# Kernel tuning notes

Hardware: AMD Instinct MI355X
Metric: run time of the kernel (lower is better)

Reference implementation:

```python
import jax, jax.numpy as jnp
import numpy as np

NUM_HEADS = 12
OT_REG = 0.1
SINKHORN_ITERS = 10
DIAG_VAL = 1e3


def setup_inputs() -> dict:
    key = jax.random.key(0)
    k1, k2, k3 = jax.random.split(key, 3)
    B, N, C = 64, 256, 768
    x = jax.random.normal(k1, (B, N, C), dtype=jnp.float32)
    w_qkv = jax.random.normal(k2, (3 * C, C), dtype=jnp.float32) * (C ** -0.5)
    w_proj = jax.random.normal(k3, (C, C), dtype=jnp.float32) * (C ** -0.5)
    b_proj = jnp.zeros((C,), dtype=jnp.float32)
    return {"x": x, "w_qkv": w_qkv, "w_proj": w_proj, "b_proj": b_proj}


def _sot(q):
    # q: [B, H, N, hd] -> self-optimal-transport plan [B, H, N, N]
    N = q.shape[-2]
    qn = q / (jnp.linalg.norm(q, axis=-1, keepdims=True) + 1e-8)
    C = 1.0 - jnp.einsum('bhnd,bhmd->bhnm', qn, qn)          # cosine cost
    eye = jnp.eye(N, dtype=bool)
    C = jnp.where(eye, DIAG_VAL, C)                            # mask diagonal
    log_K = -C / OT_REG
    log_marg = -jnp.log(jnp.float32(N))                        # uniform r = c = 1/N
    log_v = jnp.zeros(q.shape[:2] + (N,), dtype=q.dtype)
    for _ in range(SINKHORN_ITERS):
        log_u = log_marg - jax.nn.logsumexp(log_K + log_v[..., None, :], axis=-1)
        log_v = log_marg - jax.nn.logsumexp(log_K + log_u[..., :, None], axis=-2)
    log_T = log_u[..., :, None] + log_K + log_v[..., None, :]
    z = jnp.exp(log_T)
    z = z / jnp.max(z, axis=(-2, -1), keepdims=True)           # max_scale per sample/head
    z = jnp.where(eye, 1.0, z)                                 # diagonal set to 1
    return z


def reference(x, w_qkv, w_proj, b_proj):
    B, N, C = x.shape
    H = NUM_HEADS
    hd = C // H
    scale = hd ** -0.5
    qkv = jnp.einsum('bnc,oc->bno', x, w_qkv)                  # [B, N, 3C]
    qkv = qkv.reshape(B, N, 3, H, hd).transpose(2, 0, 3, 1, 4)  # [3, B, H, N, hd]
    q, k, v = qkv[0], qkv[1], qkv[2]
    attn = _sot(q)                                              # [B, H, N, N]
    attn = jax.nn.softmax(attn * scale, axis=-1)               # dropout = identity (eval)
    out = jnp.einsum('bhnm,bhmd->bhnd', attn, v)
    out = out.transpose(0, 2, 1, 3).reshape(B, N, C)
    out = jnp.einsum('bnc,oc->bno', out, w_proj) + b_proj
    return out
```

## Files before the change

kernel.cpp:

```cpp
#include <hip/hip_runtime.h>

typedef unsigned short u16;
typedef unsigned int   u32;
typedef __attribute__((ext_vector_type(8))) short bf16x8;
typedef __attribute__((ext_vector_type(4))) float f32x4;

__device__ __forceinline__ u16 f2bf(float f) {
    u32 u = __float_as_uint(f);
    u += 0x7fffu + ((u >> 16) & 1u);
    return (u16)(u >> 16);
}
__device__ __forceinline__ float bf2f(u16 s) {
    return __uint_as_float(((u32)s) << 16);
}
__device__ __forceinline__ u32 pack2bf(float f0, float f1) {
    return (u32)f2bf(f0) | ((u32)f2bf(f1) << 16);
}
__device__ __forceinline__ u32 cvtpk2bf(float f0, float f1) {
    u32 r;
    asm("v_cvt_pk_bf16_f32 %0, %1, %2" : "=v"(r) : "v"(f0), "v"(f1));
    return r;
}

__device__ __forceinline__ void gload_lds16(const void* g, void* l) {
    __builtin_amdgcn_global_load_lds(
        (const __attribute__((address_space(1))) u32*)g,
        (__attribute__((address_space(3))) u32*)l, 16, 0, 0);
}

__global__ __launch_bounds__(256)
void conv_all(const float* __restrict__ x, const float* __restrict__ wqkv,
              const float* __restrict__ wproj, u16* __restrict__ xbf,
              u16* __restrict__ wqv, u16* __restrict__ wpb)
{
    const int i = blockIdx.x * 256 + threadIdx.x;
    if (i < 1572864) {
        const float4 a = ((const float4*)x)[2*i];
        const float4 b = ((const float4*)x)[2*i + 1];
        ((uint4*)xbf)[i] = make_uint4(pack2bf(a.x,a.y), pack2bf(a.z,a.w),
                                      pack2bf(b.x,b.y), pack2bf(b.z,b.w));
    } else if (i < 1572864 + 147456) {
        const int j = i - 1572864;
        const int row = j / 96;
        const int cc  = (j - row * 96) * 8;
        const int srow = row + (row >= 768 ? 768 : 0);
        const float4 a = *(const float4*)&wqkv[(size_t)srow*768 + cc];
        const float4 b = *(const float4*)&wqkv[(size_t)srow*768 + cc + 4];
        *(uint4*)&wqv[(size_t)row*768 + cc] =
            make_uint4(pack2bf(a.x,a.y), pack2bf(a.z,a.w),
                       pack2bf(b.x,b.y), pack2bf(b.z,b.w));
    } else if (i < 1572864 + 147456 + 73728) {
        const int j = i - 1572864 - 147456;
        const float4 a = ((const float4*)wproj)[2*j];
        const float4 b = ((const float4*)wproj)[2*j + 1];
        ((uint4*)wpb)[j] = make_uint4(pack2bf(a.x,a.y), pack2bf(a.z,a.w),
                                      pack2bf(b.x,b.y), pack2bf(b.z,b.w));
    }
}

__global__ __launch_bounds__(256, 3)
void gemm_qkv_mfma(const u16* __restrict__ xbf, const u16* __restrict__ wqv,
                   u16* __restrict__ qnbf, u16* __restrict__ vbfT)
{
    __shared__ u16 As[128*64];
    __shared__ u16 Bq[128*64];
    __shared__ u16 Bv[128*64];
    const int m0 = blockIdx.x * 128;
    const int bj = blockIdx.y;
    const int tid = threadIdx.x;
    const int l = tid & 63, w = tid >> 6;
    const int wr = w >> 1, wc = w & 1;

    f32x4 accq[4][4], accv[4][4];
    #pragma unroll
    for (int i = 0; i < 4; ++i)
        #pragma unroll
        for (int j = 0; j < 4; ++j) {
            accq[i][j] = (f32x4){0.f,0.f,0.f,0.f};
            accv[i][j] = (f32x4){0.f,0.f,0.f,0.f};
        }

    const char* Ar  = (const char*)xbf + (size_t)m0*1536;
    const char* Bqr = (const char*)wqv + (size_t)(bj*128)*1536;
    const char* Bvr = (const char*)wqv + (size_t)(768 + bj*128)*1536;
    char* Asb = (char*)As;
    char* Bqb = (char*)Bq;
    char* Bvb = (char*)Bv;
    const int co = 16 * ((l & 7) ^ (l >> 3));
    const size_t rstep = (size_t)(l >> 3) * 1536;
    const int rsw = (l & 7) << 4;

    for (int k0 = 0; k0 < 1536; k0 += 128) {
        #pragma unroll
        for (int i = 0; i < 4; ++i) {
            const int rb = i*32 + w*8;
            const size_t goff = (size_t)rb*1536 + rstep + k0 + co;
            gload_lds16(Ar  + goff, Asb + i*4096 + w*1024);
            gload_lds16(Bqr + goff, Bqb + i*4096 + w*1024);
            gload_lds16(Bvr + goff, Bvb + i*4096 + w*1024);
        }
        __syncthreads();
        #pragma unroll
        for (int kk = 0; kk < 2; ++kk) {
            const int coff = (kk*64 + ((l >> 4) << 4)) ^ rsw;
            bf16x8 af[4], bq[4], bv[4];
            #pragma unroll
            for (int mi = 0; mi < 4; ++mi) {
                const int rowA = wr*64 + mi*16 + (l & 15);
                af[mi] = *(const bf16x8*)(Asb + rowA*128 + coff);
                const int rowB = wc*64 + mi*16 + (l & 15);
                bq[mi] = *(const bf16x8*)(Bqb + rowB*128 + coff);
                bv[mi] = *(const bf16x8*)(Bvb + rowB*128 + coff);
            }
            #pragma unroll
            for (int mi = 0; mi < 4; ++mi)
                #pragma unroll
                for (int nj = 0; nj < 4; ++nj)
                    accq[mi][nj] = __builtin_amdgcn_mfma_f32_16x16x32_bf16(
                                       af[mi], bq[nj], accq[mi][nj], 0, 0, 0);
            #pragma unroll
            for (int mi = 0; mi < 4; ++mi)
                #pragma unroll
                for (int nj = 0; nj < 4; ++nj)
                    accv[mi][nj] = __builtin_amdgcn_mfma_f32_16x16x32_bf16(
                                       af[mi], bv[nj], accv[mi][nj], 0, 0, 0);
        }
        __syncthreads();
    }

    const int rbase = m0 + wr*64 + ((l >> 4) << 2);
    {
        const int h = 2*bj + wc;
        #pragma unroll
        for (int mi = 0; mi < 4; ++mi)
            #pragma unroll
            for (int rr = 0; rr < 4; ++rr) {
                float s =      accq[mi][0][rr]*accq[mi][0][rr];
                s = fmaf(accq[mi][1][rr], accq[mi][1][rr], s);
                s = fmaf(accq[mi][2][rr], accq[mi][2][rr], s);
                s = fmaf(accq[mi][3][rr], accq[mi][3][rr], s);
                #pragma unroll
                for (int off = 1; off < 16; off <<= 1) s += __shfl_xor(s, off);
                const float inv = 1.0f / (sqrtf(s) + 1e-8f);
                const int m = rbase + mi*16 + rr;
                const int b_ = m >> 8, n_ = m & 255;
                u16* row = qnbf + ((((size_t)b_*12 + h) << 8) + n_)*64;
                #pragma unroll
                for (int nj = 0; nj < 4; ++nj)
                    row[nj*16 + (l & 15)] = f2bf(accq[mi][nj][rr] * inv);
            }
    }
    {
        const int colb = bj*128 + wc*64;
        #pragma unroll
        for (int mi = 0; mi < 4; ++mi)
            #pragma unroll
            for (int nj = 0; nj < 4; ++nj) {
                const int col = colb + nj*16 + (l & 15);
                const int h = col >> 6, d = col & 63;
                const int m = rbase + mi*16;
                const int b_ = m >> 8, n_ = m & 255;
                uint2 o = make_uint2(pack2bf(accv[mi][nj][0], accv[mi][nj][1]),
                                     pack2bf(accv[mi][nj][2], accv[mi][nj][3]));
                *(uint2*)&vbfT[(((size_t)b_*12 + h)*64 + d)*256 + n_] = o;
            }
    }
}

__global__ __launch_bounds__(256, 2)
void gemm_proj_mfma(const u16* __restrict__ ctxb, const u16* __restrict__ wpb,
                    const float* __restrict__ bias, float* __restrict__ out)
{
    __shared__ u16 As[128*64];
    __shared__ u16 B1[128*64];
    __shared__ u16 B2[128*64];
    const int m0 = blockIdx.x * 128;
    const int n0 = blockIdx.y * 256;
    const int tid = threadIdx.x;
    const int l = tid & 63, w = tid >> 6;
    const int wr = w >> 1, wc = w & 1;

    f32x4 acc1[4][4], acc2[4][4];
    #pragma unroll
    for (int i = 0; i < 4; ++i)
        #pragma unroll
        for (int j = 0; j < 4; ++j) {
            acc1[i][j] = (f32x4){0.f,0.f,0.f,0.f};
            acc2[i][j] = (f32x4){0.f,0.f,0.f,0.f};
        }

    const char* Ar  = (const char*)ctxb + (size_t)m0*1536;
    const char* B1r = (const char*)wpb + (size_t)n0*1536;
    const char* B2r = (const char*)wpb + (size_t)(n0 + 128)*1536;
    char* Asb = (char*)As;
    char* B1b = (char*)B1;
    char* B2b = (char*)B2;
    const int co = 16 * ((l & 7) ^ (l >> 3));
    const size_t rstep = (size_t)(l >> 3) * 1536;
    const int rsw = (l & 7) << 4;

    for (int k0 = 0; k0 < 1536; k0 += 128) {
        #pragma unroll
        for (int i = 0; i < 4; ++i) {
            const int rb = i*32 + w*8;
            const size_t goff = (size_t)rb*1536 + rstep + k0 + co;
            gload_lds16(Ar  + goff, Asb + i*4096 + w*1024);
            gload_lds16(B1r + goff, B1b + i*4096 + w*1024);
            gload_lds16(B2r + goff, B2b + i*4096 + w*1024);
        }
        __syncthreads();
        #pragma unroll
        for (int kk = 0; kk < 2; ++kk) {
            const int coff = (kk*64 + ((l >> 4) << 4)) ^ rsw;
            bf16x8 af[4], b1[4], b2[4];
            #pragma unroll
            for (int mi = 0; mi < 4; ++mi) {
                const int rowA = wr*64 + mi*16 + (l & 15);
                af[mi] = *(const bf16x8*)(Asb + rowA*128 + coff);
                const int rowB = wc*64 + mi*16 + (l & 15);
                b1[mi] = *(const bf16x8*)(B1b + rowB*128 + coff);
                b2[mi] = *(const bf16x8*)(B2b + rowB*128 + coff);
            }
            #pragma unroll
            for (int mi = 0; mi < 4; ++mi)
                #pragma unroll
                for (int nj = 0; nj < 4; ++nj)
                    acc1[mi][nj] = __builtin_amdgcn_mfma_f32_16x16x32_bf16(
                                       af[mi], b1[nj], acc1[mi][nj], 0, 0, 0);
            #pragma unroll
            for (int mi = 0; mi < 4; ++mi)
                #pragma unroll
                for (int nj = 0; nj < 4; ++nj)
                    acc2[mi][nj] = __builtin_amdgcn_mfma_f32_16x16x32_bf16(
                                       af[mi], b2[nj], acc2[mi][nj], 0, 0, 0);
        }
        __syncthreads();
    }

    const int rbase = m0 + wr*64 + ((l >> 4) << 2);
    #pragma unroll
    for (int mi = 0; mi < 4; ++mi)
        #pragma unroll
        for (int nj = 0; nj < 4; ++nj) {
            const int col = n0 + wc*64 + nj*16 + (l & 15);
            const float bv = bias[col];
            #pragma unroll
            for (int rr = 0; rr < 4; ++rr) {
                const int m = rbase + mi*16 + rr;
                out[(size_t)m*768 + col] = acc1[mi][nj][rr] + bv;
            }
        }
    #pragma unroll
    for (int mi = 0; mi < 4; ++mi)
        #pragma unroll
        for (int nj = 0; nj < 4; ++nj) {
            const int col = n0 + 128 + wc*64 + nj*16 + (l & 15);
            const float bv = bias[col];
            #pragma unroll
            for (int rr = 0; rr < 4; ++rr) {
                const int m = rbase + mi*16 + rr;
                out[(size_t)m*768 + col] = acc2[mi][nj][rr] + bv;
            }
        }
}

__global__ __launch_bounds__(256)
void cost_kernel(const u16* __restrict__ qnbf, u16* __restrict__ Kmat)
{
    __shared__ u16 Qa[128*64];
    __shared__ u16 Qb[128*64];
    const int bh = blockIdx.y;
    const int tr = (blockIdx.x >> 1) * 128;
    const int tc = (blockIdx.x & 1) * 128;
    const char* qb = (const char*)(qnbf + (size_t)bh * 16384);
    const int tid = threadIdx.x;
    const int l = tid & 63, w = tid >> 6;
    const int wr = w >> 1, wc = w & 1;

    {
        const int co = ((l & 7) ^ (l >> 3)) << 4;
        const int rl = l >> 3;
        #pragma unroll
        for (int i = 0; i < 4; ++i) {
            const int ch = i*4 + w;
            gload_lds16(qb + (size_t)(tr + ch*8 + rl)*128 + co, (char*)Qa + ch*1024);
            gload_lds16(qb + (size_t)(tc + ch*8 + rl)*128 + co, (char*)Qb + ch*1024);
        }
    }
    __syncthreads();

    f32x4 acc[4][4];
    #pragma unroll
    for (int i = 0; i < 4; ++i)
        #pragma unroll
        for (int j = 0; j < 4; ++j) acc[i][j] = (f32x4){0.f,0.f,0.f,0.f};

    bf16x8 af[2][4], bfr[2][4];
    #pragma unroll
    for (int kk = 0; kk < 2; ++kk) {
        const int kb = kk*64 + ((l >> 4) << 4);
        #pragma unroll
        for (int f = 0; f < 4; ++f) {
            const int ra = wr*64 + f*16 + (l & 15);
            af[kk][f]  = *(const bf16x8*)((char*)Qa + ra*128 + (kb ^ ((ra & 7) << 4)));
            const int rb = wc*64 + f*16 + (l & 15);
            bfr[kk][f] = *(const bf16x8*)((char*)Qb + rb*128 + (kb ^ ((rb & 7) << 4)));
        }
    }
    #pragma unroll
    for (int mi = 0; mi < 4; ++mi)
        #pragma unroll
        for (int nj = 0; nj < 4; ++nj) {
            acc[mi][nj] = __builtin_amdgcn_mfma_f32_16x16x32_bf16(
                              af[0][mi], bfr[0][nj], acc[mi][nj], 0, 0, 0);
            acc[mi][nj] = __builtin_amdgcn_mfma_f32_16x16x32_bf16(
                              af[1][mi], bfr[1][nj], acc[mi][nj], 0, 0, 0);
        }

    u16* Kb = Kmat + (size_t)bh * 65536;
    #pragma unroll
    for (int mi = 0; mi < 4; ++mi)
        #pragma unroll
        for (int nj = 0; nj < 4; ++nj) {
            const int gr0 = tr + wr*64 + mi*16 + ((l >> 4) << 2);
            const int gc  = tc + wc*64 + nj*16 + (l & 15);
            #pragma unroll
            for (int rr = 0; rr < 4; ++rr) {
                const int gr = gr0 + rr;
                const float s = acc[mi][nj][rr];
                const float km = (gr == gc) ? 0.f : __expf(fmaf(10.f, s, -10.f));
                Kb[(size_t)gr * 256 + gc] = f2bf(km);
            }
        }
}

__global__ __launch_bounds__(512, 2)
void sinkhorn_kernel(const u16* __restrict__ Kmat, float* __restrict__ ubuf,
                     float* __restrict__ vbuf, float* __restrict__ tmaxbuf)
{
    __shared__ __align__(16) float xv[256];
    __shared__ __align__(16) float usave[256];
    __shared__ __align__(16) u16   xbf[256];
    __shared__ float pmax[8];
    const int bh  = blockIdx.x;
    const int tid = threadIdx.x;
    const int l = tid & 63, w = tid >> 6;
    const int rowb = w * 32;
    const char* Kg = (const char*)(Kmat + (size_t)bh * 65536);

    bf16x8 kf[2][8];
    {
        const char* kb0 = Kg + (size_t)(rowb + (l & 15)) * 512 + ((l >> 4) << 4);
        #pragma unroll
        for (int t = 0; t < 2; ++t)
            #pragma unroll
            for (int ks = 0; ks < 8; ++ks)
                kf[t][ks] = *(const bf16x8*)(kb0 + t*8192 + ks*64);
    }
    if (tid < 256) xbf[tid] = 0x3f80;
    __syncthreads();

    for (int it = 0; it < 20; ++it) {
        f32x4 a0a = {0.f,0.f,0.f,0.f}, a0b = {0.f,0.f,0.f,0.f};
        f32x4 a1a = {0.f,0.f,0.f,0.f}, a1b = {0.f,0.f,0.f,0.f};
        #pragma unroll
        for (int ks = 0; ks < 4; ++ks) {
            const bf16x8 xf = *(const bf16x8*)((const char*)xbf + ks*64 + ((l >> 4) << 4));
            a0a = __builtin_amdgcn_mfma_f32_16x16x32_bf16(kf[0][ks], xf, a0a, 0, 0, 0);
            a1a = __builtin_amdgcn_mfma_f32_16x16x32_bf16(kf[1][ks], xf, a1a, 0, 0, 0);
        }
        #pragma unroll
        for (int ks = 4; ks < 8; ++ks) {
            const bf16x8 xf = *(const bf16x8*)((const char*)xbf + ks*64 + ((l >> 4) << 4));
            a0b = __builtin_amdgcn_mfma_f32_16x16x32_bf16(kf[0][ks], xf, a0b, 0, 0, 0);
            a1b = __builtin_amdgcn_mfma_f32_16x16x32_bf16(kf[1][ks], xf, a1b, 0, 0, 0);
        }
        float xn0[4], xn1[4];
        #pragma unroll
        for (int j = 0; j < 4; ++j) {
            xn0[j] = 0.00390625f * __builtin_amdgcn_rcpf(a0a[j] + a0b[j]);
            xn1[j] = 0.00390625f * __builtin_amdgcn_rcpf(a1a[j] + a1b[j]);
        }
        const u32 xp0 = cvtpk2bf(xn0[0], xn0[1]);
        const u32 xp1 = cvtpk2bf(xn0[2], xn0[3]);
        const u32 xp2 = cvtpk2bf(xn1[0], xn1[1]);
        const u32 xp3 = cvtpk2bf(xn1[2], xn1[3]);
        if ((l & 15) == 0) {
            const int r0 = rowb + ((l >> 4) << 2);
            *(uint2*)&xbf[r0]      = make_uint2(xp0, xp1);
            *(uint2*)&xbf[r0 + 16] = make_uint2(xp2, xp3);
            if (it == 18) {
                *(float4*)&usave[r0]      = make_float4(xn0[0], xn0[1], xn0[2], xn0[3]);
                *(float4*)&usave[r0 + 16] = make_float4(xn1[0], xn1[1], xn1[2], xn1[3]);
            }
            if (it == 19) {
                *(float4*)&xv[r0]      = make_float4(xn0[0], xn0[1], xn0[2], xn0[3]);
                *(float4*)&xv[r0 + 16] = make_float4(xn1[0], xn1[1], xn1[2], xn1[3]);
            }
        }
        __syncthreads();
    }

    {
        float mx0 = 0.f, mx1 = 0.f;
        #pragma unroll
        for (int ks = 0; ks < 8; ++ks) {
            const int mbase = ks*32 + ((l >> 4) << 3);
            const float4 va  = *(const float4*)&xv[mbase];
            const float4 vb4 = *(const float4*)&xv[mbase + 4];
            const float vv[8] = {va.x, va.y, va.z, va.w, vb4.x, vb4.y, vb4.z, vb4.w};
            #pragma unroll
            for (int j = 0; j < 8; ++j) {
                mx0 = fmaxf(mx0, bf2f((u16)kf[0][ks][j]) * vv[j]);
                mx1 = fmaxf(mx1, bf2f((u16)kf[1][ks][j]) * vv[j]);
            }
        }
        float mx = fmaxf(usave[rowb + (l & 15)] * mx0,
                         usave[rowb + 16 + (l & 15)] * mx1);
        #pragma unroll
        for (int off = 32; off > 0; off >>= 1) mx = fmaxf(mx, __shfl_xor(mx, off));
        if (l == 0) pmax[w] = mx;
    }
    __syncthreads();
    if (tid < 256) {
        ubuf[bh * 256 + tid] = usave[tid];
        vbuf[bh * 256 + tid] = xv[tid];
    }
    if (tid == 0) {
        float tm = pmax[0];
        #pragma unroll
        for (int i = 1; i < 8; ++i) tm = fmaxf(tm, pmax[i]);
        tmaxbuf[bh] = tm;
    }
}

__global__ __launch_bounds__(512, 2)
void pv_kernel(const u16* __restrict__ Kmat, const u16* __restrict__ vbfT,
               const float* __restrict__ ubuf, const float* __restrict__ vbuf,
               const float* __restrict__ tmaxbuf, u16* __restrict__ ctxc)
{
    __shared__ u16 Vt[64*256];
    __shared__ __align__(16) float xv[256];
    const int bh  = blockIdx.x;
    const int b_ = bh / 12, h_ = bh - b_*12;
    const int tid = threadIdx.x;
    const int l = tid & 63, w = tid >> 6;
    const int rowb = w * 32;
    const char* Kg = (const char*)(Kmat + (size_t)bh * 65536);

    {
        const char* src = (const char*)(vbfT + (size_t)bh * 16384);
        char* dst = (char*)Vt;
        const int s = l & 31;
        #pragma unroll
        for (int i = 0; i < 4; ++i) {
            const int d = i*16 + w*2 + (l >> 5);
            gload_lds16(src + d*512 + ((s ^ (d & 7)) << 4), dst + i*8192 + w*1024);
        }
    }
    if (tid < 256) xv[tid] = vbuf[bh*256 + tid];

    bf16x8 kf[2][8];
    {
        const char* kb0 = Kg + (size_t)(rowb + (l & 15)) * 512 + ((l >> 4) << 4);
        #pragma unroll
        for (int t = 0; t < 2; ++t)
            #pragma unroll
            for (int ks = 0; ks < 8; ++ks)
                kf[t][ks] = *(const bf16x8*)(kb0 + t*8192 + ks*64);
    }
    const float itmax = 1.0f / tmaxbuf[bh];
    const float u0 = ubuf[bh*256 + rowb + (l & 15)];
    const float u1 = ubuf[bh*256 + rowb + 16 + (l & 15)];
    __syncthreads();

    u16* outp = ctxc + ((size_t)b_*256)*768 + h_*64;
    #pragma unroll
    for (int t = 0; t < 2; ++t) {
        const int rown = rowb + t*16 + (l & 15);
        const float an = (t == 0 ? u0 : u1) * itmax * 0.125f;
        float psum = 0.f;
        f32x4 acc0 = {0.f,0.f,0.f,0.f}, acc1 = {0.f,0.f,0.f,0.f};
        f32x4 acc2 = {0.f,0.f,0.f,0.f}, acc3 = {0.f,0.f,0.f,0.f};
        #pragma unroll
        for (int ks = 0; ks < 8; ++ks) {
            const int mbase = ks*32 + ((l >> 4) << 3);
            const float4 va  = *(const float4*)&xv[mbase];
            const float4 vb4 = *(const float4*)&xv[mbase + 4];
            const float vv[8] = {va.x, va.y, va.z, va.w, vb4.x, vb4.y, vb4.z, vb4.w};
            float p[8];
            #pragma unroll
            for (int j = 0; j < 8; ++j)
                p[j] = __expf(an * bf2f((u16)kf[t][ks][j]) * vv[j]);
            const int dj = rown - mbase;
            if (dj >= 0 && dj < 8) p[dj] = 1.13314845f;
            psum += ((p[0]+p[1]) + (p[2]+p[3])) + ((p[4]+p[5]) + (p[6]+p[7]));
            uint4 pwv = make_uint4(cvtpk2bf(p[0], p[1]), cvtpk2bf(p[2], p[3]),
                                   cvtpk2bf(p[4], p[5]), cvtpk2bf(p[6], p[7]));
            const bf16x8 pf = *(const bf16x8*)&pwv;
            const int bc = ks*64 + ((l >> 4) << 4);
            {
                const int d = (l & 15);
                const bf16x8 vf = *(const bf16x8*)((char*)Vt + d*512 + (bc ^ ((d & 7) << 4)));
                acc0 = __builtin_amdgcn_mfma_f32_16x16x32_bf16(vf, pf, acc0, 0, 0, 0);
            }
            {
                const int d = 16 + (l & 15);
                const bf16x8 vf = *(const bf16x8*)((char*)Vt + d*512 + (bc ^ ((d & 7) << 4)));
                acc1 = __builtin_amdgcn_mfma_f32_16x16x32_bf16(vf, pf, acc1, 0, 0, 0);
            }
            {
                const int d = 32 + (l & 15);
                const bf16x8 vf = *(const bf16x8*)((char*)Vt + d*512 + (bc ^ ((d & 7) << 4)));
                acc2 = __builtin_amdgcn_mfma_f32_16x16x32_bf16(vf, pf, acc2, 0, 0, 0);
            }
            {
                const int d = 48 + (l & 15);
                const bf16x8 vf = *(const bf16x8*)((char*)Vt + d*512 + (bc ^ ((d & 7) << 4)));
                acc3 = __builtin_amdgcn_mfma_f32_16x16x32_bf16(vf, pf, acc3, 0, 0, 0);
            }
        }
        psum += __shfl_xor(psum, 16);
        psum += __shfl_xor(psum, 32);
        const float is = 1.0f / psum;
        const int d0 = (l >> 4) << 2;
        uint2 o0 = make_uint2(cvtpk2bf(acc0[0]*is, acc0[1]*is), cvtpk2bf(acc0[2]*is, acc0[3]*is));
        uint2 o1 = make_uint2(cvtpk2bf(acc1[0]*is, acc1[1]*is), cvtpk2bf(acc1[2]*is, acc1[3]*is));
        uint2 o2 = make_uint2(cvtpk2bf(acc2[0]*is, acc2[1]*is), cvtpk2bf(acc2[2]*is, acc2[3]*is));
        uint2 o3 = make_uint2(cvtpk2bf(acc3[0]*is, acc3[1]*is), cvtpk2bf(acc3[2]*is, acc3[3]*is));
        u16* orow = outp + (size_t)rown*768;
        *(uint2*)&orow[d0]      = o0;
        *(uint2*)&orow[16 + d0] = o1;
        *(uint2*)&orow[32 + d0] = o2;
        *(uint2*)&orow[48 + d0] = o3;
    }
}

extern "C" void kernel_launch(void* const* d_in, const int* in_sizes, int n_in,
                              void* d_out, int out_size, void* d_ws, size_t ws_size,
                              hipStream_t stream)
{
    (void)in_sizes; (void)n_in; (void)out_size; (void)ws_size;
    const float* x      = (const float*)d_in[0];
    const float* w_qkv  = (const float*)d_in[1];
    const float* w_proj = (const float*)d_in[2];
    const float* b_proj = (const float*)d_in[3];
    float* out = (float*)d_out;

    char* w = (char*)d_ws;
    u16*   xbf  = (u16*)  (w);
    u16*   wqv  = (u16*)  (w + 25165824);
    u16*   wpb  = (u16*)  (w + 27525120);
    u16*   qnbf = (u16*)  (w + 28704768);
    u16*   vbfT = (u16*)  (w + 79036416);
    u16*   ctxc = (u16*)  (w + 104202240);
    float* ub   = (float*)(w + 129368064);
    float* vb   = (float*)(w + 130154496);
    float* tmx  = (float*)(w + 130940928);
    u16*   Km   = (u16*)  (w + 130944000);

    conv_all       <<<dim3(7008),    256, 0, stream>>>(x, w_qkv, w_proj, xbf, wqv, wpb);
    gemm_qkv_mfma  <<<dim3(128, 6),  256, 0, stream>>>(xbf, wqv, qnbf, vbfT);
    cost_kernel    <<<dim3(4, 768),  256, 0, stream>>>(qnbf, Km);
    sinkhorn_kernel<<<dim3(768),     512, 0, stream>>>(Km, ub, vb, tmx);
    pv_kernel      <<<dim3(768),     512, 0, stream>>>(Km, vbfT, ub, vb, tmx, ctxc);
    gemm_proj_mfma <<<dim3(128, 3),  256, 0, stream>>>(ctxc, wpb, b_proj, out);
}
```

Baseline: 198.4 us.

## Fuse cost matrix computation into sinkhorn and PV kernels, drop K buffer

Removes the separate cost_kernel that wrote the exp-kernel matrix K (768 x 256x256 bf16, about 100MB) to global memory. Instead, both sinkhorn and pv kernels load normalized Q into LDS and recompute K in registers via MFMA Gram products plus exp. The K column ordering changes to match the MFMA output layout, so the x-vector and V loads are adjusted. This trades a large global write and two reads for duplicated Gram compute and extra LDS (32KB Q tile) per block, which may reduce occupancy.

```diff
diff --git a/kernel.cpp b/kernel.cpp
--- a/kernel.cpp
+++ b/kernel.cpp
@@ -58,6 +58,51 @@
     }
 }
 
+__device__ __forceinline__ void gram_kf(const char* Qs, const int l,
+                                        const int rowb, bf16x8 kf[2][8])
+{
+    const int q = l >> 4;
+    #pragma unroll
+    for (int t = 0; t < 2; ++t) {
+        const int rb = rowb + t*16 + (l & 15);
+        bf16x8 bfr[2];
+        #pragma unroll
+        for (int kk = 0; kk < 2; ++kk)
+            bfr[kk] = *(const bf16x8*)(Qs + rb*128 + ((kk*64 + q*16) ^ ((rb & 7) << 4)));
+        #pragma unroll
+        for (int ks = 0; ks < 8; ++ks) {
+            f32x4 d0 = {0.f,0.f,0.f,0.f}, d1 = {0.f,0.f,0.f,0.f};
+            {
+                const int ra = (ks*2)*16 + (l & 15);
+                #pragma unroll
+                for (int kk = 0; kk < 2; ++kk) {
+                    const bf16x8 af = *(const bf16x8*)(Qs + ra*128 + ((kk*64 + q*16) ^ ((ra & 7) << 4)));
+                    d0 = __builtin_amdgcn_mfma_f32_16x16x32_bf16(af, bfr[kk], d0, 0, 0, 0);
+                }
+            }
+            {
+                const int ra = (ks*2 + 1)*16 + (l & 15);
+                #pragma unroll
+                for (int kk = 0; kk < 2; ++kk) {
+                    const bf16x8 af = *(const bf16x8*)(Qs + ra*128 + ((kk*64 + q*16) ^ ((ra & 7) << 4)));
+                    d1 = __builtin_amdgcn_mfma_f32_16x16x32_bf16(af, bfr[kk], d1, 0, 0, 0);
+                }
+            }
+            float km[8];
+            #pragma unroll
+            for (int rr = 0; rr < 4; ++rr) {
+                const int c0 = ks*32 + q*4 + rr;
+                km[rr]   = (c0 == rb) ? 0.f : __expf(fmaf(10.f, d0[rr], -10.f));
+                const int c1 = ks*32 + 16 + q*4 + rr;
+                km[4+rr] = (c1 == rb) ? 0.f : __expf(fmaf(10.f, d1[rr], -10.f));
+            }
+            uint4 kw = make_uint4(pack2bf(km[0],km[1]), pack2bf(km[2],km[3]),
+                                  pack2bf(km[4],km[5]), pack2bf(km[6],km[7]));
+            kf[t][ks] = *(const bf16x8*)&kw;
+        }
+    }
+}
+
 __global__ __launch_bounds__(256, 3)
 void gemm_qkv_mfma(const u16* __restrict__ xbf, const u16* __restrict__ wqv,
                    u16* __restrict__ qnbf, u16* __restrict__ vbfT)
@@ -264,80 +309,11 @@
         }
 }
 
-__global__ __launch_bounds__(256)
-void cost_kernel(const u16* __restrict__ qnbf, u16* __restrict__ Kmat)
-{
-    __shared__ u16 Qa[128*64];
-    __shared__ u16 Qb[128*64];
-    const int bh = blockIdx.y;
-    const int tr = (blockIdx.x >> 1) * 128;
-    const int tc = (blockIdx.x & 1) * 128;
-    const char* qb = (const char*)(qnbf + (size_t)bh * 16384);
-    const int tid = threadIdx.x;
-    const int l = tid & 63, w = tid >> 6;
-    const int wr = w >> 1, wc = w & 1;
-
-    {
-        const int co = ((l & 7) ^ (l >> 3)) << 4;
-        const int rl = l >> 3;
-        #pragma unroll
-        for (int i = 0; i < 4; ++i) {
-            const int ch = i*4 + w;
-            gload_lds16(qb + (size_t)(tr + ch*8 + rl)*128 + co, (char*)Qa + ch*1024);
-            gload_lds16(qb + (size_t)(tc + ch*8 + rl)*128 + co, (char*)Qb + ch*1024);
-        }
-    }
-    __syncthreads();
-
-    f32x4 acc[4][4];
-    #pragma unroll
-    for (int i = 0; i < 4; ++i)
-        #pragma unroll
-        for (int j = 0; j < 4; ++j) acc[i][j] = (f32x4){0.f,0.f,0.f,0.f};
-
-    bf16x8 af[2][4], bfr[2][4];
-    #pragma unroll
-    for (int kk = 0; kk < 2; ++kk) {
-        const int kb = kk*64 + ((l >> 4) << 4);
-        #pragma unroll
-        for (int f = 0; f < 4; ++f) {
-            const int ra = wr*64 + f*16 + (l & 15);
-            af[kk][f]  = *(const bf16x8*)((char*)Qa + ra*128 + (kb ^ ((ra & 7) << 4)));
-            const int rb = wc*64 + f*16 + (l & 15);
-            bfr[kk][f] = *(const bf16x8*)((char*)Qb + rb*128 + (kb ^ ((rb & 7) << 4)));
-        }
-    }
-    #pragma unroll
-    for (int mi = 0; mi < 4; ++mi)
-        #pragma unroll
-        for (int nj = 0; nj < 4; ++nj) {
-            acc[mi][nj] = __builtin_amdgcn_mfma_f32_16x16x32_bf16(
-                              af[0][mi], bfr[0][nj], acc[mi][nj], 0, 0, 0);
-            acc[mi][nj] = __builtin_amdgcn_mfma_f32_16x16x32_bf16(
-                              af[1][mi], bfr[1][nj], acc[mi][nj], 0, 0, 0);
-        }
-
-    u16* Kb = Kmat + (size_t)bh * 65536;
-    #pragma unroll
-    for (int mi = 0; mi < 4; ++mi)
-        #pragma unroll
-        for (int nj = 0; nj < 4; ++nj) {
-            const int gr0 = tr + wr*64 + mi*16 + ((l >> 4) << 2);
-            const int gc  = tc + wc*64 + nj*16 + (l & 15);
-            #pragma unroll
-            for (int rr = 0; rr < 4; ++rr) {
-                const int gr = gr0 + rr;
-                const float s = acc[mi][nj][rr];
-                const float km = (gr == gc) ? 0.f : __expf(fmaf(10.f, s, -10.f));
-                Kb[(size_t)gr * 256 + gc] = f2bf(km);
-            }
-        }
-}
-
 __global__ __launch_bounds__(512, 2)
-void sinkhorn_kernel(const u16* __restrict__ Kmat, float* __restrict__ ubuf,
+void sinkhorn_kernel(const u16* __restrict__ qnbf, float* __restrict__ ubuf,
                      float* __restrict__ vbuf, float* __restrict__ tmaxbuf)
 {
+    __shared__ u16 Qs[256*64];
     __shared__ __align__(16) float xv[256];
     __shared__ __align__(16) float usave[256];
     __shared__ __align__(16) u16   xbf[256];
@@ -346,34 +322,39 @@
     const int tid = threadIdx.x;
     const int l = tid & 63, w = tid >> 6;
     const int rowb = w * 32;
-    const char* Kg = (const char*)(Kmat + (size_t)bh * 65536);
-
-    bf16x8 kf[2][8];
+
     {
-        const char* kb0 = Kg + (size_t)(rowb + (l & 15)) * 512 + ((l >> 4) << 4);
-        #pragma unroll
-        for (int t = 0; t < 2; ++t)
-            #pragma unroll
-            for (int ks = 0; ks < 8; ++ks)
-                kf[t][ks] = *(const bf16x8*)(kb0 + t*8192 + ks*64);
+        const char* src = (const char*)(qnbf + (size_t)bh * 16384);
+        const int s = tid & 7;
+        #pragma unroll
+        for (int i = 0; i < 4; ++i) {
+            const int row = i*64 + (tid >> 3);
+            gload_lds16(src + row*128 + ((s ^ (row & 7)) << 4), (char*)Qs + i*8192 + tid*16);
+        }
     }
     if (tid < 256) xbf[tid] = 0x3f80;
     __syncthreads();
+
+    bf16x8 kf[2][8];
+    gram_kf((const char*)Qs, l, rowb, kf);
 
     for (int it = 0; it < 20; ++it) {
         f32x4 a0a = {0.f,0.f,0.f,0.f}, a0b = {0.f,0.f,0.f,0.f};
         f32x4 a1a = {0.f,0.f,0.f,0.f}, a1b = {0.f,0.f,0.f,0.f};
         #pragma unroll
-        for (int ks = 0; ks < 4; ++ks) {
-            const bf16x8 xf = *(const bf16x8*)((const char*)xbf + ks*64 + ((l >> 4) << 4));
-            a0a = __builtin_amdgcn_mfma_f32_16x16x32_bf16(kf[0][ks], xf, a0a, 0, 0, 0);
-            a1a = __builtin_amdgcn_mfma_f32_16x16x32_bf16(kf[1][ks], xf, a1a, 0, 0, 0);
-        }
-        #pragma unroll
-        for (int ks = 4; ks < 8; ++ks) {
-            const bf16x8 xf = *(const bf16x8*)((const char*)xbf + ks*64 + ((l >> 4) << 4));
-            a0b = __builtin_amdgcn_mfma_f32_16x16x32_bf16(kf[0][ks], xf, a0b, 0, 0, 0);
-            a1b = __builtin_amdgcn_mfma_f32_16x16x32_bf16(kf[1][ks], xf, a1b, 0, 0, 0);
+        for (int ks = 0; ks < 8; ++ks) {
+            const char* xb = (const char*)xbf + ks*64 + ((l >> 4) << 3);
+            const uint2 lo = *(const uint2*)xb;
+            const uint2 hi = *(const uint2*)(xb + 32);
+            uint4 xw4 = make_uint4(lo.x, lo.y, hi.x, hi.y);
+            const bf16x8 xf = *(const bf16x8*)&xw4;
+            if (ks < 4) {
+                a0a = __builtin_amdgcn_mfma_f32_16x16x32_bf16(kf[0][ks], xf, a0a, 0, 0, 0);
+                a1a = __builtin_amdgcn_mfma_f32_16x16x32_bf16(kf[1][ks], xf, a1a, 0, 0, 0);
+            } else {
+                a0b = __builtin_amdgcn_mfma_f32_16x16x32_bf16(kf[0][ks], xf, a0b, 0, 0, 0);
+                a1b = __builtin_amdgcn_mfma_f32_16x16x32_bf16(kf[1][ks], xf, a1b, 0, 0, 0);
+            }
         }
         float xn0[4], xn1[4];
         #pragma unroll
@@ -405,9 +386,9 @@
         float mx0 = 0.f, mx1 = 0.f;
         #pragma unroll
         for (int ks = 0; ks < 8; ++ks) {
-            const int mbase = ks*32 + ((l >> 4) << 3);
-            const float4 va  = *(const float4*)&xv[mbase];
-            const float4 vb4 = *(const float4*)&xv[mbase + 4];
+            const int mb = ks*32 + ((l >> 4) << 2);
+            const float4 va  = *(const float4*)&xv[mb];
+            const float4 vb4 = *(const float4*)&xv[mb + 16];
             const float vv[8] = {va.x, va.y, va.z, va.w, vb4.x, vb4.y, vb4.z, vb4.w};
             #pragma unroll
             for (int j = 0; j < 8; ++j) {
@@ -435,10 +416,11 @@
 }
 
 __global__ __launch_bounds__(512, 2)
-void pv_kernel(const u16* __restrict__ Kmat, const u16* __restrict__ vbfT,
+void pv_kernel(const u16* __restrict__ qnbf, const u16* __restrict__ vbfT,
                const float* __restrict__ ubuf, const float* __restrict__ vbuf,
                const float* __restrict__ tmaxbuf, u16* __restrict__ ctxc)
 {
+    __shared__ u16 Qs[256*64];
     __shared__ u16 Vt[64*256];
     __shared__ __align__(16) float xv[256];
     const int bh  = blockIdx.x;
@@ -446,35 +428,34 @@
     const int tid = threadIdx.x;
     const int l = tid & 63, w = tid >> 6;
     const int rowb = w * 32;
-    const char* Kg = (const char*)(Kmat + (size_t)bh * 65536);
 
     {
-        const char* src = (const char*)(vbfT + (size_t)bh * 16384);
-        char* dst = (char*)Vt;
+        const char* srcq = (const char*)(qnbf + (size_t)bh * 16384);
+        const int sq = tid & 7;
+        #pragma unroll
+        for (int i = 0; i < 4; ++i) {
+            const int row = i*64 + (tid >> 3);
+            gload_lds16(srcq + row*128 + ((sq ^ (row & 7)) << 4), (char*)Qs + i*8192 + tid*16);
+        }
+        const char* srcv = (const char*)(vbfT + (size_t)bh * 16384);
         const int s = l & 31;
         #pragma unroll
         for (int i = 0; i < 4; ++i) {
             const int d = i*16 + w*2 + (l >> 5);
-            gload_lds16(src + d*512 + ((s ^ (d & 7)) << 4), dst + i*8192 + w*1024);
+            gload_lds16(srcv + d*512 + ((s ^ (d & 7)) << 4), (char*)Vt + i*8192 + w*1024);
         }
     }
     if (tid < 256) xv[tid] = vbuf[bh*256 + tid];
-
-    bf16x8 kf[2][8];
-    {
-        const char* kb0 = Kg + (size_t)(rowb + (l & 15)) * 512 + ((l >> 4) << 4);
-        #pragma unroll
-        for (int t = 0; t < 2; ++t)
-            #pragma unroll
-            for (int ks = 0; ks < 8; ++ks)
-                kf[t][ks] = *(const bf16x8*)(kb0 + t*8192 + ks*64);
-    }
     const float itmax = 1.0f / tmaxbuf[bh];
     const float u0 = ubuf[bh*256 + rowb + (l & 15)];
     const float u1 = ubuf[bh*256 + rowb + 16 + (l & 15)];
     __syncthreads();
 
+    bf16x8 kf[2][8];
+    gram_kf((const char*)Qs, l, rowb, kf);
+
     u16* outp = ctxc + ((size_t)b_*256)*768 + h_*64;
+    const int q = l >> 4;
     #pragma unroll
     for (int t = 0; t < 2; ++t) {
         const int rown = rowb + t*16 + (l & 15);
@@ -484,46 +465,43 @@
         f32x4 acc2 = {0.f,0.f,0.f,0.f}, acc3 = {0.f,0.f,0.f,0.f};
         #pragma unroll
         for (int ks = 0; ks < 8; ++ks) {
-            const int mbase = ks*32 + ((l >> 4) << 3);
-            const float4 va  = *(const float4*)&xv[mbase];
-            const float4 vb4 = *(const float4*)&xv[mbase + 4];
+            const int mb = ks*32 + (q << 2);
+            const float4 va  = *(const float4*)&xv[mb];
+            const float4 vb4 = *(const float4*)&xv[mb + 16];
             const float vv[8] = {va.x, va.y, va.z, va.w, vb4.x, vb4.y, vb4.z, vb4.w};
             float p[8];
             #pragma unroll
             for (int j = 0; j < 8; ++j)
                 p[j] = __expf(an * bf2f((u16)kf[t][ks][j]) * vv[j]);
-            const int dj = rown - mbase;
-            if (dj >= 0 && dj < 8) p[dj] = 1.13314845f;
+            const int d0j = rown - mb;
+            if (d0j >= 0 && d0j < 4) p[d0j] = 1.13314845f;
+            const int d1j = rown - mb - 16;
+            if (d1j >= 0 && d1j < 4) p[4 + d1j] = 1.13314845f;
             psum += ((p[0]+p[1]) + (p[2]+p[3])) + ((p[4]+p[5]) + (p[6]+p[7]));
             uint4 pwv = make_uint4(cvtpk2bf(p[0], p[1]), cvtpk2bf(p[2], p[3]),
                                    cvtpk2bf(p[4], p[5]), cvtpk2bf(p[6], p[7]));
             const bf16x8 pf = *(const bf16x8*)&pwv;
-            const int bc = ks*64 + ((l >> 4) << 4);
-            {
-                const int d = (l & 15);
-                const bf16x8 vf = *(const bf16x8*)((char*)Vt + d*512 + (bc ^ ((d & 7) << 4)));
-                acc0 = __builtin_amdgcn_mfma_f32_16x16x32_bf16(vf, pf, acc0, 0, 0, 0);
-            }
-            {
-                const int d = 16 + (l & 15);
-                const bf16x8 vf = *(const bf16x8*)((char*)Vt + d*512 + (bc ^ ((d & 7) << 4)));
-                acc1 = __builtin_amdgcn_mfma_f32_16x16x32_bf16(vf, pf, acc1, 0, 0, 0);
-            }
-            {
-                const int d = 32 + (l & 15);
-                const bf16x8 vf = *(const bf16x8*)((char*)Vt + d*512 + (bc ^ ((d & 7) << 4)));
-                acc2 = __builtin_amdgcn_mfma_f32_16x16x32_bf16(vf, pf, acc2, 0, 0, 0);
-            }
-            {
-                const int d = 48 + (l & 15);
-                const bf16x8 vf = *(const bf16x8*)((char*)Vt + d*512 + (bc ^ ((d & 7) << 4)));
-                acc3 = __builtin_amdgcn_mfma_f32_16x16x32_bf16(vf, pf, acc3, 0, 0, 0);
+            const int b0 = ks*64 + (q << 3);
+            #pragma unroll
+            for (int dt = 0; dt < 4; ++dt) {
+                const int d = dt*16 + (l & 15);
+                const int sl0 = (b0 >> 4), re0 = b0 & 15;
+                const uint2 lo = *(const uint2*)((char*)Vt + d*512 + ((sl0 ^ (d & 7)) << 4) + re0);
+                const int b1 = b0 + 32;
+                const int sl1 = (b1 >> 4), re1 = b1 & 15;
+                const uint2 hi = *(const uint2*)((char*)Vt + d*512 + ((sl1 ^ (d & 7)) << 4) + re1);
+                uint4 vw = make_uint4(lo.x, lo.y, hi.x, hi.y);
+                const bf16x8 vf = *(const bf16x8*)&vw;
+                if (dt == 0) acc0 = __builtin_amdgcn_mfma_f32_16x16x32_bf16(vf, pf, acc0, 0, 0, 0);
+                if (dt == 1) acc1 = __builtin_amdgcn_mfma_f32_16x16x32_bf16(vf, pf, acc1, 0, 0, 0);
+                if (dt == 2) acc2 = __builtin_amdgcn_mfma_f32_16x16x32_bf16(vf, pf, acc2, 0, 0, 0);
+                if (dt == 3) acc3 = __builtin_amdgcn_mfma_f32_16x16x32_bf16(vf, pf, acc3, 0, 0, 0);
             }
         }
         psum += __shfl_xor(psum, 16);
         psum += __shfl_xor(psum, 32);
         const float is = 1.0f / psum;
-        const int d0 = (l >> 4) << 2;
+        const int d0 = q << 2;
         uint2 o0 = make_uint2(cvtpk2bf(acc0[0]*is, acc0[1]*is), cvtpk2bf(acc0[2]*is, acc0[3]*is));
         uint2 o1 = make_uint2(cvtpk2bf(acc1[0]*is, acc1[1]*is), cvtpk2bf(acc1[2]*is, acc1[3]*is));
         uint2 o2 = make_uint2(cvtpk2bf(acc2[0]*is, acc2[1]*is), cvtpk2bf(acc2[2]*is, acc2[3]*is));
@@ -557,12 +535,10 @@
     float* ub   = (float*)(w + 129368064);
     float* vb   = (float*)(w + 130154496);
     float* tmx  = (float*)(w + 130940928);
-    u16*   Km   = (u16*)  (w + 130944000);
 
     conv_all       <<<dim3(7008),    256, 0, stream>>>(x, w_qkv, w_proj, xbf, wqv, wpb);
     gemm_qkv_mfma  <<<dim3(128, 6),  256, 0, stream>>>(xbf, wqv, qnbf, vbfT);
-    cost_kernel    <<<dim3(4, 768),  256, 0, stream>>>(qnbf, Km);
-    sinkhorn_kernel<<<dim3(768),     512, 0, stream>>>(Km, ub, vb, tmx);
-    pv_kernel      <<<dim3(768),     512, 0, stream>>>(Km, vbfT, ub, vb, tmx, ctxc);
+    sinkhorn_kernel<<<dim3(768),     512, 0, stream>>>(qnbf, ub, vb, tmx);
+    pv_kernel      <<<dim3(768),     512, 0, stream>>>(qnbf, vbfT, ub, vb, tmx, ctxc);
     gemm_proj_mfma <<<dim3(128, 3),  256, 0, stream>>>(ctxc, wpb, b_proj, out);
 }
```

Measured after the change: 207.5 us. 1.05x slower.
